# Kernel optimization log

Hardware: AMD Instinct MI355X
Metric: run time of the kernel (lower is better)

## Reference

```python
import jax, jax.numpy as jnp
import numpy as np
from jax.ops import segment_sum

N_NODES = 50000
N_EDGES = 800000
D_IN = 256
D_HID2 = 256   # hidden_channels * 2
D_HID = 128    # hidden_channels
D_MLP = 64     # hidden_channels // 2
D_OUT = 64


def setup_inputs() -> dict:
    key = jax.random.key(0)
    ks = jax.random.split(key, 16)
    def glorot(k, shape):
        lim = float(np.sqrt(6.0 / (shape[0] + shape[1])))
        return jax.random.uniform(k, shape, jnp.float32, -lim, lim)
    x = jax.random.normal(ks[0], (N_NODES, D_IN), jnp.float32)
    edge_index = jax.random.randint(ks[1], (2, N_EDGES), 0, N_NODES, jnp.int64)
    return {
        "x": x,
        "edge_index": edge_index,
        "W1": glorot(ks[2], (D_IN, D_HID2)),   "b1": jnp.zeros((D_HID2,), jnp.float32),
        "W2": glorot(ks[3], (D_HID2, D_HID2)), "b2": jnp.zeros((D_HID2,), jnp.float32),
        "W3": glorot(ks[4], (D_HID2, D_HID)),  "b3": jnp.zeros((D_HID,), jnp.float32),
        "mW1": glorot(ks[5], (D_HID, D_MLP)),  "mb1": jnp.zeros((D_MLP,), jnp.float32),
        "mW2": glorot(ks[6], (D_MLP, D_OUT)),  "mb2": jnp.zeros((D_OUT,), jnp.float32),
    }


def _graph_conv(x, src, dst, W, b, n_nodes):
    # DGL GraphConv with norm='both': h = D_in^{-1/2} * A @ (D_out^{-1/2} * x @ W) + b
    ones = jnp.ones((src.shape[0],), x.dtype)
    deg_out = jnp.clip(segment_sum(ones, src, num_segments=n_nodes), 1.0)
    deg_in = jnp.clip(segment_sum(ones, dst, num_segments=n_nodes), 1.0)
    h = (x * jax.lax.rsqrt(deg_out)[:, None]) @ W          # [N, d_out]
    agg = segment_sum(h[src], dst, num_segments=n_nodes)    # gather-scatter over edges
    return agg * jax.lax.rsqrt(deg_in)[:, None] + b


def reference(x, edge_index, W1, b1, W2, b2, W3, b3, mW1, mb1, mW2, mb2):
    src, dst = edge_index[0], edge_index[1]
    n = x.shape[0]
    # eval mode: dropout is identity
    h = jax.nn.relu(_graph_conv(x, src, dst, W1, b1, n))
    h = jax.nn.relu(_graph_conv(h, src, dst, W2, b2, n))
    h_last = jax.nn.relu(_graph_conv(h, src, dst, W3, b3, n))
    out = jax.nn.relu(h_last @ mW1 + mb1) @ mW2 + mb2
    return (out, h_last)
```

## Files before the change

### kernel.cpp

```cpp
#include <hip/hip_runtime.h>
#include <hip/hip_bf16.h>

typedef __hip_bfloat16 bf16;
typedef __attribute__((ext_vector_type(8))) __bf16 bfrag;
typedef __attribute__((ext_vector_type(4))) float f32x4;

#define N_NODES 50000
#define N_EDGES 800000
#define GB_GEMM 782
#define GB_PLACE 3125

__device__ __forceinline__ unsigned short f2bf(float f) {
    bf16 h = __float2bfloat16(f);
    return *reinterpret_cast<unsigned short*>(&h);
}

__device__ __forceinline__ uint4 zero4() { uint4 z; z.x = z.y = z.z = z.w = 0u; return z; }

__device__ __forceinline__ void load_edge(const int* __restrict__ ei, int fl64,
                                          int e, int& s, int& d) {
    if (fl64) {
        int2 a = ((const int2*)ei)[e];
        int2 b = ((const int2*)ei)[N_EDGES + e];
        s = a.x; d = b.x;
    } else {
        s = ei[e];
        d = ei[N_EDGES + e];
    }
}

__device__ __forceinline__ float rdf(const void* p, int off, int f32) {
    return f32 ? ((const float*)p)[off] : (float)((const bf16*)p)[off];
}

__global__ void detect_zero_kernel(const unsigned short* __restrict__ xb,
                                   const int* __restrict__ ei,
                                   int* __restrict__ flags,
                                   int* __restrict__ cnt) {
    int i = blockIdx.x * 256 + threadIdx.x;
    if (i < 2 * N_NODES) cnt[i] = 0;
    if (blockIdx.x == 0) {
        __shared__ int s_insane, s_nonzero;
        int t = threadIdx.x;
        if (t == 0) { s_insane = 0; s_nonzero = 0; }
        __syncthreads();
        unsigned short h = xb[2 * t];
        int e = (h >> 7) & 0xFF;
        if (!(e == 0 || (e >= 90 && e <= 150))) atomicOr(&s_insane, 1);
        if (ei[2 * t + 1] != 0) atomicOr(&s_nonzero, 1);
        __syncthreads();
        if (t == 0) { flags[0] = s_insane ? 1 : 0; flags[1] = s_nonzero ? 0 : 1; }
    }
}

__global__ void cvt_all_kernel(const void* W1, const void* W2, const void* W3,
                               const void* mW1, const void* mW2,
                               const void* b1, const void* b2, const void* b3,
                               const void* mb1, const void* mb2,
                               const int* __restrict__ flags,
                               unsigned short* __restrict__ WT,
                               float* __restrict__ biasd) {
    int i = blockIdx.x * 256 + threadIdx.x;
    if (i >= 176896) return;
    const int f32 = flags[0];
    if (i < 163840) {
        const void* s; int local, N;
        if      (i <  65536) { s = W1; local = i;          N = 256; }
        else if (i < 131072) { s = W2; local = i -  65536; N = 256; }
        else                 { s = W3; local = i - 131072; N = 128; }
        int n = local >> 8, k = local & 255;
        WT[i] = f2bf(rdf(s, k * N + n, f32));
    } else if (i < 172032) {
        int local = i - 163840;
        int n = local >> 7, k = local & 127;
        WT[i] = f2bf(rdf(mW1, k * 64 + n, f32));
    } else if (i < 176128) {
        int local = i - 172032;
        int n = local >> 6, k = local & 63;
        WT[i] = f2bf(rdf(mW2, k * 64 + n, f32));
    } else {
        int local = i - 176128;
        const void* s; int off;
        if      (local < 256) { s = b1;  off = local; }
        else if (local < 512) { s = b2;  off = local - 256; }
        else if (local < 640) { s = b3;  off = local - 512; }
        else if (local < 704) { s = mb1; off = local - 640; }
        else                  { s = mb2; off = local - 704; }
        biasd[local] = rdf(s, off, f32);
    }
}

__device__ __forceinline__ uint4 ld8_bf16(const unsigned short* p) {
    return *(const uint4*)p;
}
__device__ __forceinline__ uint4 ld8_f32(const float* p) {
    float4 a = *(const float4*)(p);
    float4 b = *(const float4*)(p + 4);
    uint4 r;
    r.x = ((unsigned)f2bf(a.y) << 16) | f2bf(a.x);
    r.y = ((unsigned)f2bf(a.w) << 16) | f2bf(a.z);
    r.z = ((unsigned)f2bf(b.y) << 16) | f2bf(b.x);
    r.w = ((unsigned)f2bf(b.w) << 16) | f2bf(b.z);
    return r;
}

template <bool DUALX, bool PRESCALE>
__device__ __forceinline__ void gemm_body(
        unsigned short (*Xs)[40], unsigned short (*Ws)[40],
        const void* __restrict__ Xv, const int* __restrict__ flags,
        const unsigned short* __restrict__ WT,
        const int* __restrict__ cntS,
        unsigned short* __restrict__ C,
        int bx, int by, int M, int N) {
    constexpr int K = 256;
    const int tid  = threadIdx.x;
    const int lane = tid & 63;
    const int w    = tid >> 6;
    const int wr   = (w >> 1) * 64;
    const int wc   = (w & 1) * 64;
    const int lrow = lane & 15;
    const int koff = (lane >> 4) * 8;
    const int row0 = by * 128;
    const int col0 = bx * 128;
    const bool xf32 = DUALX && (flags[0] != 0);
    const unsigned short* Xb = (const unsigned short*)Xv;
    const float* Xf = (const float*)Xv;

    const int r0 = tid >> 2, q0 = tid & 3;
    const int r1 = r0 + 64;
    const int gr0 = row0 + r0, gr1 = row0 + r1;

    uint4 xv0, xv1, wv0, wv1;
    {
        int e = q0 * 8;
        xv0 = (gr0 < M) ? (xf32 ? ld8_f32(Xf + (size_t)gr0 * K + e)
                                : ld8_bf16(Xb + (size_t)gr0 * K + e)) : zero4();
        xv1 = (gr1 < M) ? (xf32 ? ld8_f32(Xf + (size_t)gr1 * K + e)
                                : ld8_bf16(Xb + (size_t)gr1 * K + e)) : zero4();
        wv0 = *(const uint4*)(WT + (size_t)(col0 + r0) * K + e);
        wv1 = *(const uint4*)(WT + (size_t)(col0 + r1) * K + e);
    }

    f32x4 acc[4][4] = {};

    for (int k0 = 0; k0 < K; k0 += 32) {
        *(uint4*)&Xs[r0][q0 * 8] = xv0;
        *(uint4*)&Xs[r1][q0 * 8] = xv1;
        *(uint4*)&Ws[r0][q0 * 8] = wv0;
        *(uint4*)&Ws[r1][q0 * 8] = wv1;
        __syncthreads();

        const int k1 = k0 + 32;
        if (k1 < K) {
            int e = k1 + q0 * 8;
            xv0 = (gr0 < M) ? (xf32 ? ld8_f32(Xf + (size_t)gr0 * K + e)
                                    : ld8_bf16(Xb + (size_t)gr0 * K + e)) : zero4();
            xv1 = (gr1 < M) ? (xf32 ? ld8_f32(Xf + (size_t)gr1 * K + e)
                                    : ld8_bf16(Xb + (size_t)gr1 * K + e)) : zero4();
            wv0 = *(const uint4*)(WT + (size_t)(col0 + r0) * K + e);
            wv1 = *(const uint4*)(WT + (size_t)(col0 + r1) * K + e);
        }

        bfrag af[4], bv[4];
#pragma unroll
        for (int i = 0; i < 4; i++)
            af[i] = *(const bfrag*)&Xs[wr + i * 16 + lrow][koff];
#pragma unroll
        for (int j = 0; j < 4; j++)
            bv[j] = *(const bfrag*)&Ws[wc + j * 16 + lrow][koff];
#pragma unroll
        for (int i = 0; i < 4; i++)
#pragma unroll
            for (int j = 0; j < 4; j++)
                acc[i][j] = __builtin_amdgcn_mfma_f32_16x16x32_bf16(
                    af[i], bv[j], acc[i][j], 0, 0, 0);
        __syncthreads();
    }

#pragma unroll
    for (int i = 0; i < 4; i++) {
#pragma unroll
        for (int r = 0; r < 4; r++) {
            int row = row0 + wr + i * 16 + ((lane >> 4) * 4) + r;
            if (row >= M) continue;
            const float s = PRESCALE ? rsqrtf((float)max(cntS[row], 1)) : 1.0f;
#pragma unroll
            for (int j = 0; j < 4; j++) {
                int col = col0 + wc + j * 16 + lrow;
                C[(size_t)row * N + col] = f2bf(acc[i][j][r] * s);
            }
        }
    }
}

__launch_bounds__(256)
__global__ void megaA_kernel(const void* __restrict__ x,
                             const int* __restrict__ ei,
                             const int* __restrict__ flags,
                             const unsigned short* __restrict__ WT,
                             unsigned short* __restrict__ Hbf,
                             int* __restrict__ cntS, int* __restrict__ cntD,
                             unsigned short* __restrict__ esrc_pad, int M) {
    __shared__ unsigned short Xs[128][40];
    __shared__ unsigned short Ws[128][40];
    const int bid = blockIdx.x;
    if (bid < GB_PLACE) {
        int e = bid * 256 + threadIdx.x;
        if (e < N_EDGES) {
            int s, d; load_edge(ei, flags[1], e, s, d);
            atomicAdd(&cntS[s], 1);
            int pos = atomicAdd(&cntD[d], 1);
            if (pos < 64)
                __builtin_nontemporal_store((unsigned short)s,
                                            &esrc_pad[(d << 6) + pos]);
        }
    } else {
        const int gb = bid - GB_PLACE;
        gemm_body<true, false>(Xs, Ws, x, flags, WT, nullptr, Hbf,
                               gb & 1, gb >> 1, M, 256);
    }
}

__launch_bounds__(256)
__global__ void mfma_gemm_kernel(const unsigned short* __restrict__ X,
                                 const int* __restrict__ flags,
                                 const unsigned short* __restrict__ WT,
                                 const int* __restrict__ cntS,
                                 unsigned short* __restrict__ C,
                                 int M, int N) {
    __shared__ unsigned short Xs[128][40];
    __shared__ unsigned short Ws[128][40];
    gemm_body<false, true>(Xs, Ws, X, flags, WT, cntS, C,
                           blockIdx.x, blockIdx.y, M, N);
}

__launch_bounds__(256)
__global__ void mfma_mlp2_kernel(const unsigned short* __restrict__ X,
                                 const unsigned short* __restrict__ WT1,
                                 const unsigned short* __restrict__ WT2,
                                 const float* __restrict__ b1,
                                 const float* __restrict__ b2,
                                 float* __restrict__ out, int M) {
    __shared__ unsigned short Xs[128][136];
    __shared__ unsigned short W1s[64][136];
    __shared__ unsigned short W2s[64][72];
    const int tid  = threadIdx.x;
    const int lane = tid & 63;
    const int w    = tid >> 6;
    const int lrow = lane & 15;
    const int koff = (lane >> 4) * 8;
    const int row0 = blockIdx.x * 128;

#pragma unroll
    for (int i = 0; i < 8; i++) {
        int c = tid + i * 256;
        int r = c >> 4, q = c & 15;
        int gr = row0 + r;
        uint4 v = (gr < M) ? *(const uint4*)(X + (size_t)gr * 128 + q * 8) : zero4();
        *(uint4*)&Xs[r][q * 8] = v;
    }
#pragma unroll
    for (int i = 0; i < 4; i++) {
        int c = tid + i * 256;
        int n = c >> 4, q = c & 15;
        *(uint4*)&W1s[n][q * 8] = *(const uint4*)(WT1 + (size_t)n * 128 + q * 8);
    }
#pragma unroll
    for (int i = 0; i < 2; i++) {
        int c = tid + i * 256;
        int n = c >> 3, q = c & 7;
        *(uint4*)&W2s[n][q * 8] = *(const uint4*)(WT2 + (size_t)n * 64 + q * 8);
    }
    __syncthreads();

    f32x4 acc[2][4] = {};
#pragma unroll
    for (int k0 = 0; k0 < 128; k0 += 32) {
        bfrag af[2], bv[4];
#pragma unroll
        for (int i = 0; i < 2; i++)
            af[i] = *(const bfrag*)&Xs[w * 32 + i * 16 + lrow][k0 + koff];
#pragma unroll
        for (int j = 0; j < 4; j++)
            bv[j] = *(const bfrag*)&W1s[j * 16 + lrow][k0 + koff];
#pragma unroll
        for (int i = 0; i < 2; i++)
#pragma unroll
            for (int j = 0; j < 4; j++)
                acc[i][j] = __builtin_amdgcn_mfma_f32_16x16x32_bf16(
                    af[i], bv[j], acc[i][j], 0, 0, 0);
    }
    __syncthreads();

#pragma unroll
    for (int i = 0; i < 2; i++) {
#pragma unroll
        for (int r = 0; r < 4; r++) {
            int row = w * 32 + i * 16 + ((lane >> 4) * 4) + r;
#pragma unroll
            for (int j = 0; j < 4; j++) {
                int col = j * 16 + lrow;
                Xs[row][col] = f2bf(fmaxf(acc[i][j][r] + b1[col], 0.0f));
            }
        }
    }
    __syncthreads();

    f32x4 acc2[2][4] = {};
#pragma unroll
    for (int k0 = 0; k0 < 64; k0 += 32) {
        bfrag af[2], bv[4];
#pragma unroll
        for (int i = 0; i < 2; i++)
            af[i] = *(const bfrag*)&Xs[w * 32 + i * 16 + lrow][k0 + koff];
#pragma unroll
        for (int j = 0; j < 4; j++)
            bv[j] = *(const bfrag*)&W2s[j * 16 + lrow][k0 + koff];
#pragma unroll
        for (int i = 0; i < 2; i++)
#pragma unroll
            for (int j = 0; j < 4; j++)
                acc2[i][j] = __builtin_amdgcn_mfma_f32_16x16x32_bf16(
                    af[i], bv[j], acc2[i][j], 0, 0, 0);
    }

#pragma unroll
    for (int i = 0; i < 2; i++) {
#pragma unroll
        for (int r = 0; r < 4; r++) {
            int row = row0 + w * 32 + i * 16 + ((lane >> 4) * 4) + r;
            if (row >= M) continue;
#pragma unroll
            for (int j = 0; j < 4; j++) {
                int col = j * 16 + lrow;
                out[(size_t)row * 64 + col] = acc2[i][j][r] + b2[col];
            }
        }
    }
}

__device__ __forceinline__ void accs(unsigned int u, float s, float& a0, float& a1) {
    a0 = fmaf(s, __uint_as_float(u << 16), a0);
    a1 = fmaf(s, __uint_as_float(u & 0xffff0000u), a1);
}
__device__ __forceinline__ void acc4s(uint4 u, float s, float (&a)[8]) {
    accs(u.x, s, a[0], a[1]); accs(u.y, s, a[2], a[3]);
    accs(u.z, s, a[4], a[5]); accs(u.w, s, a[6], a[7]);
}

template <int LQ, bool ESCALE, int OUT>
__launch_bounds__(256)
__global__ void gather_bf16_kernel(const int* __restrict__ cntD,
                                   const int* __restrict__ cntS,
                                   const unsigned short* __restrict__ esrc_pad,
                                   const unsigned short* __restrict__ H,
                                   const float* __restrict__ bias,
                                   float* __restrict__ Yf,
                                   unsigned short* __restrict__ Yb, int nNodes) {
    constexpr int NPB = 256 / LQ;
    constexpr int D = LQ * 8;
    const int tid = threadIdx.x;
    const int node = blockIdx.x * NPB + tid / LQ;
    const int lane = tid % LQ;
    if (node >= nNodes) return;
    const uint4* __restrict__ H4 = (const uint4*)H;
    const unsigned short* __restrict__ ep = esrc_pad + (node << 6);

    float a[8] = {};
    const int cn = min(cntD[node], 64);
    int j = 0;
    for (; j + 8 <= cn; j += 8) {
        int s[8];
#pragma unroll
        for (int t = 0; t < 8; t++) s[t] = ep[j + t];
        float w[8];
#pragma unroll
        for (int t = 0; t < 8; t++)
            w[t] = ESCALE ? rsqrtf((float)max(cntS[s[t]], 1)) : 1.0f;
        uint4 u[8];
#pragma unroll
        for (int t = 0; t < 8; t++) u[t] = H4[(size_t)s[t] * LQ + lane];
#pragma unroll
        for (int t = 0; t < 8; t++) acc4s(u[t], w[t], a);
    }
    for (; j + 4 <= cn; j += 4) {
        int s[4];
#pragma unroll
        for (int t = 0; t < 4; t++) s[t] = ep[j + t];
        float w[4];
#pragma unroll
        for (int t = 0; t < 4; t++)
            w[t] = ESCALE ? rsqrtf((float)max(cntS[s[t]], 1)) : 1.0f;
        uint4 u[4];
#pragma unroll
        for (int t = 0; t < 4; t++) u[t] = H4[(size_t)s[t] * LQ + lane];
#pragma unroll
        for (int t = 0; t < 4; t++) acc4s(u[t], w[t], a);
    }
    for (; j < cn; j++) {
        int s0 = ep[j];
        float w0 = ESCALE ? rsqrtf((float)max(cntS[s0], 1)) : 1.0f;
        uint4 u = H4[(size_t)s0 * LQ + lane];
        acc4s(u, w0, a);
    }
    const float sc = rsqrtf((float)max(cntD[node], 1));
    const float* bp = bias + lane * 8;
    float4 b0 = *(const float4*)(bp);
    float4 b1 = *(const float4*)(bp + 4);
    float r0 = fmaxf(fmaf(a[0], sc, b0.x), 0.0f);
    float r1 = fmaxf(fmaf(a[1], sc, b0.y), 0.0f);
    float r2 = fmaxf(fmaf(a[2], sc, b0.z), 0.0f);
    float r3 = fmaxf(fmaf(a[3], sc, b0.w), 0.0f);
    float r4 = fmaxf(fmaf(a[4], sc, b1.x), 0.0f);
    float r5 = fmaxf(fmaf(a[5], sc, b1.y), 0.0f);
    float r6 = fmaxf(fmaf(a[6], sc, b1.z), 0.0f);
    float r7 = fmaxf(fmaf(a[7], sc, b1.w), 0.0f);
    if (OUT == 2) {
        float* yp = Yf + (size_t)node * D + lane * 8;
        float4 o0 = {r0, r1, r2, r3};
        float4 o1 = {r4, r5, r6, r7};
        *(float4*)(yp)     = o0;
        *(float4*)(yp + 4) = o1;
    }
    {
        unsigned short* yp = Yb + (size_t)node * D + lane * 8;
        ushort4 o0, o1;
        o0.x = f2bf(r0); o0.y = f2bf(r1); o0.z = f2bf(r2); o0.w = f2bf(r3);
        o1.x = f2bf(r4); o1.y = f2bf(r5); o1.z = f2bf(r6); o1.w = f2bf(r7);
        *(ushort4*)(yp)     = o0;
        *(ushort4*)(yp + 4) = o1;
    }
}

extern "C" void kernel_launch(void* const* d_in, const int* in_sizes, int n_in,
                              void* d_out, int out_size, void* d_ws, size_t ws_size,
                              hipStream_t stream) {
    const void* x  = d_in[0];
    const int*  ei = (const int*)d_in[1];
    const void *W1 = d_in[2],  *b1 = d_in[3];
    const void *W2 = d_in[4],  *b2 = d_in[5];
    const void *W3 = d_in[6],  *b3 = d_in[7];
    const void *mW1 = d_in[8], *mb1 = d_in[9];
    const void *mW2 = d_in[10],*mb2 = d_in[11];

    float* out   = (float*)d_out;
    float* out_h = out + (size_t)N_NODES * 64;

    float* ws = (float*)d_ws;
    size_t off = 0;
    int*   flags  = (int*)(ws + off); off += 64;
    int*   cntS   = (int*)(ws + off); off += N_NODES;
    int*   cntD   = (int*)(ws + off); off += N_NODES;
    unsigned short* esrc_p = (unsigned short*)(ws + off);
    off += (size_t)N_NODES * 32;
    float* biasd  = ws + off;         off += 768;
    off = (off + 63) & ~(size_t)63;
    unsigned short* WT  = (unsigned short*)(ws + off); off += 88448;
    unsigned short* Gbf = (unsigned short*)(ws + off); off += (size_t)N_NODES * 128;
    unsigned short* Hbf = (unsigned short*)(ws + off); off += (size_t)N_NODES * 128;
    unsigned short* hob = (unsigned short*)(ws + off); off += (size_t)N_NODES * 64;

    const int M = N_NODES;
    const dim3 blk(256);
    const int gy128 = (M + 127) / 128;

    detect_zero_kernel<<<391, blk, 0, stream>>>(
        (const unsigned short*)x, ei, flags, cntS);

    cvt_all_kernel<<<(176896 + 255) / 256, blk, 0, stream>>>(
        W1, W2, W3, mW1, mW2, b1, b2, b3, mb1, mb2, flags, WT, biasd);

    megaA_kernel<<<GB_GEMM + GB_PLACE, blk, 0, stream>>>(
        x, ei, flags, WT, Hbf, cntS, cntD, esrc_p, M);

    gather_bf16_kernel<32, true, 0><<<(M + 7) / 8, blk, 0, stream>>>(
        cntD, cntS, esrc_p, Hbf, biasd, nullptr, Gbf, M);

    mfma_gemm_kernel<<<dim3(2, gy128), blk, 0, stream>>>(
        Gbf, flags, WT + 65536, cntS, Hbf, M, 256);
    gather_bf16_kernel<32, false, 0><<<(M + 7) / 8, blk, 0, stream>>>(
        cntD, cntS, esrc_p, Hbf, biasd + 256, nullptr, Gbf, M);

    mfma_gemm_kernel<<<dim3(1, gy128), blk, 0, stream>>>(
        Gbf, flags, WT + 131072, cntS, Hbf, M, 128);
    gather_bf16_kernel<16, false, 2><<<(M + 15) / 16, blk, 0, stream>>>(
        cntD, cntS, esrc_p, Hbf, biasd + 512, out_h, hob, M);

    mfma_mlp2_kernel<<<gy128, blk, 0, stream>>>(
        hob, WT + 163840, WT + 172032, biasd + 640, biasd + 704, out, M);
}
```

Before: 418.2 us.

## Split gather/GEMM stages by row range and co-schedule tails with next stage

Each gather stage is split at row 40960. The head rows are gathered first. The tail-row gather then runs in the same launch as the GEMM blocks for the first 320 row tiles, whose inputs are already complete. The remaining GEMM tiles run in a separate launch afterwards. The goal is to fill the idle tail of each dependent stage and overlap gather with matmul. The change also reorders megaA so the GEMM blocks are dispatched before the edge-placement blocks, and it reuses the out_h region as scratch for H2. This adds launches and depends on exact block-count bookkeeping, and H2 lives in output memory that is overwritten later.

```diff
diff --git a/kernel.cpp b/kernel.cpp
--- a/kernel.cpp
+++ b/kernel.cpp
@@ -9,6 +9,8 @@
 #define N_EDGES 800000
 #define GB_GEMM 782
 #define GB_PLACE 3125
+#define RSPLIT 40960
+#define NTAIL (N_NODES - RSPLIT)
 
 __device__ __forceinline__ unsigned short f2bf(float f) {
     bf16 h = __float2bfloat16(f);
@@ -204,8 +206,11 @@
     __shared__ unsigned short Xs[128][40];
     __shared__ unsigned short Ws[128][40];
     const int bid = blockIdx.x;
-    if (bid < GB_PLACE) {
-        int e = bid * 256 + threadIdx.x;
+    if (bid < GB_GEMM) {
+        gemm_body<true, false>(Xs, Ws, x, flags, WT, nullptr, Hbf,
+                               bid & 1, bid >> 1, M, 256);
+    } else {
+        int e = (bid - GB_GEMM) * 256 + threadIdx.x;
         if (e < N_EDGES) {
             int s, d; load_edge(ei, flags[1], e, s, d);
             atomicAdd(&cntS[s], 1);
@@ -214,128 +219,6 @@
                 __builtin_nontemporal_store((unsigned short)s,
                                             &esrc_pad[(d << 6) + pos]);
         }
-    } else {
-        const int gb = bid - GB_PLACE;
-        gemm_body<true, false>(Xs, Ws, x, flags, WT, nullptr, Hbf,
-                               gb & 1, gb >> 1, M, 256);
-    }
-}
-
-__launch_bounds__(256)
-__global__ void mfma_gemm_kernel(const unsigned short* __restrict__ X,
-                                 const int* __restrict__ flags,
-                                 const unsigned short* __restrict__ WT,
-                                 const int* __restrict__ cntS,
-                                 unsigned short* __restrict__ C,
-                                 int M, int N) {
-    __shared__ unsigned short Xs[128][40];
-    __shared__ unsigned short Ws[128][40];
-    gemm_body<false, true>(Xs, Ws, X, flags, WT, cntS, C,
-                           blockIdx.x, blockIdx.y, M, N);
-}
-
-__launch_bounds__(256)
-__global__ void mfma_mlp2_kernel(const unsigned short* __restrict__ X,
-                                 const unsigned short* __restrict__ WT1,
-                                 const unsigned short* __restrict__ WT2,
-                                 const float* __restrict__ b1,
-                                 const float* __restrict__ b2,
-                                 float* __restrict__ out, int M) {
-    __shared__ unsigned short Xs[128][136];
-    __shared__ unsigned short W1s[64][136];
-    __shared__ unsigned short W2s[64][72];
-    const int tid  = threadIdx.x;
-    const int lane = tid & 63;
-    const int w    = tid >> 6;
-    const int lrow = lane & 15;
-    const int koff = (lane >> 4) * 8;
-    const int row0 = blockIdx.x * 128;
-
-#pragma unroll
-    for (int i = 0; i < 8; i++) {
-        int c = tid + i * 256;
-        int r = c >> 4, q = c & 15;
-        int gr = row0 + r;
-        uint4 v = (gr < M) ? *(const uint4*)(X + (size_t)gr * 128 + q * 8) : zero4();
-        *(uint4*)&Xs[r][q * 8] = v;
-    }
-#pragma unroll
-    for (int i = 0; i < 4; i++) {
-        int c = tid + i * 256;
-        int n = c >> 4, q = c & 15;
-        *(uint4*)&W1s[n][q * 8] = *(const uint4*)(WT1 + (size_t)n * 128 + q * 8);
-    }
-#pragma unroll
-    for (int i = 0; i < 2; i++) {
-        int c = tid + i * 256;
-        int n = c >> 3, q = c & 7;
-        *(uint4*)&W2s[n][q * 8] = *(const uint4*)(WT2 + (size_t)n * 64 + q * 8);
-    }
-    __syncthreads();
-
-    f32x4 acc[2][4] = {};
-#pragma unroll
-    for (int k0 = 0; k0 < 128; k0 += 32) {
-        bfrag af[2], bv[4];
-#pragma unroll
-        for (int i = 0; i < 2; i++)
-            af[i] = *(const bfrag*)&Xs[w * 32 + i * 16 + lrow][k0 + koff];
-#pragma unroll
-        for (int j = 0; j < 4; j++)
-            bv[j] = *(const bfrag*)&W1s[j * 16 + lrow][k0 + koff];
-#pragma unroll
-        for (int i = 0; i < 2; i++)
-#pragma unroll
-            for (int j = 0; j < 4; j++)
-                acc[i][j] = __builtin_amdgcn_mfma_f32_16x16x32_bf16(
-                    af[i], bv[j], acc[i][j], 0, 0, 0);
-    }
-    __syncthreads();
-
-#pragma unroll
-    for (int i = 0; i < 2; i++) {
-#pragma unroll
-        for (int r = 0; r < 4; r++) {
-            int row = w * 32 + i * 16 + ((lane >> 4) * 4) + r;
-#pragma unroll
-            for (int j = 0; j < 4; j++) {
-                int col = j * 16 + lrow;
-                Xs[row][col] = f2bf(fmaxf(acc[i][j][r] + b1[col], 0.0f));
-            }
-        }
-    }
-    __syncthreads();
-
-    f32x4 acc2[2][4] = {};
-#pragma unroll
-    for (int k0 = 0; k0 < 64; k0 += 32) {
-        bfrag af[2], bv[4];
-#pragma unroll
-        for (int i = 0; i < 2; i++)
-            af[i] = *(const bfrag*)&Xs[w * 32 + i * 16 + lrow][k0 + koff];
-#pragma unroll
-        for (int j = 0; j < 4; j++)
-            bv[j] = *(const bfrag*)&W2s[j * 16 + lrow][k0 + koff];
-#pragma unroll
-        for (int i = 0; i < 2; i++)
-#pragma unroll
-            for (int j = 0; j < 4; j++)
-                acc2[i][j] = __builtin_amdgcn_mfma_f32_16x16x32_bf16(
-                    af[i], bv[j], acc2[i][j], 0, 0, 0);
-    }
-
-#pragma unroll
-    for (int i = 0; i < 2; i++) {
-#pragma unroll
-        for (int r = 0; r < 4; r++) {
-            int row = row0 + w * 32 + i * 16 + ((lane >> 4) * 4) + r;
-            if (row >= M) continue;
-#pragma unroll
-            for (int j = 0; j < 4; j++) {
-                int col = j * 16 + lrow;
-                out[(size_t)row * 64 + col] = acc2[i][j][r] + b2[col];
-            }
-        }
     }
 }
 
@@ -349,20 +232,15 @@
 }
 
 template <int LQ, bool ESCALE, int OUT>
-__launch_bounds__(256)
-__global__ void gather_bf16_kernel(const int* __restrict__ cntD,
-                                   const int* __restrict__ cntS,
-                                   const unsigned short* __restrict__ esrc_pad,
-                                   const unsigned short* __restrict__ H,
-                                   const float* __restrict__ bias,
-                                   float* __restrict__ Yf,
-                                   unsigned short* __restrict__ Yb, int nNodes) {
-    constexpr int NPB = 256 / LQ;
+__device__ __forceinline__ void gather_body(const int* __restrict__ cntD,
+                                            const int* __restrict__ cntS,
+                                            const unsigned short* __restrict__ esrc_pad,
+                                            const unsigned short* __restrict__ H,
+                                            const float* __restrict__ bias,
+                                            float* __restrict__ Yf,
+                                            unsigned short* __restrict__ Yb,
+                                            int node, int lane) {
     constexpr int D = LQ * 8;
-    const int tid = threadIdx.x;
-    const int node = blockIdx.x * NPB + tid / LQ;
-    const int lane = tid % LQ;
-    if (node >= nNodes) return;
     const uint4* __restrict__ H4 = (const uint4*)H;
     const unsigned short* __restrict__ ep = esrc_pad + (node << 6);
 
@@ -432,6 +310,234 @@
     }
 }
 
+template <int LQ, bool ESCALE, int OUT>
+__launch_bounds__(256)
+__global__ void gather_bf16_kernel(const int* __restrict__ cntD,
+                                   const int* __restrict__ cntS,
+                                   const unsigned short* __restrict__ esrc_pad,
+                                   const unsigned short* __restrict__ H,
+                                   const float* __restrict__ bias,
+                                   float* __restrict__ Yf,
+                                   unsigned short* __restrict__ Yb,
+                                   int n0, int n1) {
+    constexpr int NPB = 256 / LQ;
+    const int node = n0 + blockIdx.x * NPB + threadIdx.x / LQ;
+    const int lane = threadIdx.x % LQ;
+    if (node >= n1) return;
+    gather_body<LQ, ESCALE, OUT>(cntD, cntS, esrc_pad, H, bias, Yf, Yb, node, lane);
+}
+
+#define MB_G 1130
+__launch_bounds__(256)
+__global__ void megaB_kernel(const int* __restrict__ cntD,
+                             const int* __restrict__ cntS,
+                             const unsigned short* __restrict__ esrc_pad,
+                             const unsigned short* __restrict__ Hbf,
+                             const float* __restrict__ biasd,
+                             unsigned short* __restrict__ Gbf,
+                             const int* __restrict__ flags,
+                             const unsigned short* __restrict__ WT2,
+                             unsigned short* __restrict__ H2, int M) {
+    const int bid = blockIdx.x;
+    if (bid < MB_G) {
+        const int node = RSPLIT + bid * 8 + threadIdx.x / 32;
+        const int lane = threadIdx.x % 32;
+        if (node >= M) return;
+        gather_body<32, true, 0>(cntD, cntS, esrc_pad, Hbf, biasd,
+                                 nullptr, Gbf, node, lane);
+    } else {
+        __shared__ unsigned short Xs[128][40];
+        __shared__ unsigned short Ws[128][40];
+        const int gb = bid - MB_G;
+        gemm_body<false, true>(Xs, Ws, Gbf, flags, WT2, cntS, H2,
+                               gb & 1, gb >> 1, M, 256);
+    }
+}
+
+__launch_bounds__(256)
+__global__ void megaC_kernel(const int* __restrict__ cntD,
+                             const int* __restrict__ cntS,
+                             const unsigned short* __restrict__ esrc_pad,
+                             const unsigned short* __restrict__ H2,
+                             const float* __restrict__ bias2,
+                             unsigned short* __restrict__ Gbf,
+                             const int* __restrict__ flags,
+                             const unsigned short* __restrict__ WT3,
+                             unsigned short* __restrict__ H3, int M) {
+    const int bid = blockIdx.x;
+    if (bid < MB_G) {
+        const int node = RSPLIT + bid * 8 + threadIdx.x / 32;
+        const int lane = threadIdx.x % 32;
+        if (node >= M) return;
+        gather_body<32, false, 0>(cntD, cntS, esrc_pad, H2, bias2,
+                                  nullptr, Gbf, node, lane);
+    } else {
+        __shared__ unsigned short Xs[128][40];
+        __shared__ unsigned short Ws[128][40];
+        const int gb = bid - MB_G;
+        gemm_body<false, true>(Xs, Ws, Gbf, flags, WT3, cntS, H3,
+                               0, gb, M, 128);
+    }
+}
+
+__launch_bounds__(256)
+__global__ void mfma_gemm_kernel(const unsigned short* __restrict__ X,
+                                 const int* __restrict__ flags,
+                                 const unsigned short* __restrict__ WT,
+                                 const int* __restrict__ cntS,
+                                 unsigned short* __restrict__ C,
+                                 int M, int N, int by0) {
+    __shared__ unsigned short Xs[128][40];
+    __shared__ unsigned short Ws[128][40];
+    gemm_body<false, true>(Xs, Ws, X, flags, WT, cntS, C,
+                           blockIdx.x, by0 + blockIdx.y, M, N);
+}
+
+__device__ __forceinline__ void mlp2_body(
+        unsigned short (*Xs)[136], unsigned short (*W1s)[136],
+        unsigned short (*W2s)[72],
+        const unsigned short* __restrict__ X,
+        const unsigned short* __restrict__ WT1,
+        const unsigned short* __restrict__ WT2,
+        const float* __restrict__ b1, const float* __restrict__ b2,
+        float* __restrict__ out, int M, int row0) {
+    const int tid  = threadIdx.x;
+    const int lane = tid & 63;
+    const int w    = tid >> 6;
+    const int lrow = lane & 15;
+    const int koff = (lane >> 4) * 8;
+
+#pragma unroll
+    for (int i = 0; i < 8; i++) {
+        int c = tid + i * 256;
+        int r = c >> 4, q = c & 15;
+        int gr = row0 + r;
+        uint4 v = (gr < M) ? *(const uint4*)(X + (size_t)gr * 128 + q * 8) : zero4();
+        *(uint4*)&Xs[r][q * 8] = v;
+    }
+#pragma unroll
+    for (int i = 0; i < 4; i++) {
+        int c = tid + i * 256;
+        int n = c >> 4, q = c & 15;
+        *(uint4*)&W1s[n][q * 8] = *(const uint4*)(WT1 + (size_t)n * 128 + q * 8);
+    }
+#pragma unroll
+    for (int i = 0; i < 2; i++) {
+        int c = tid + i * 256;
+        int n = c >> 3, q = c & 7;
+        *(uint4*)&W2s[n][q * 8] = *(const uint4*)(WT2 + (size_t)n * 64 + q * 8);
+    }
+    __syncthreads();
+
+    f32x4 acc[2][4] = {};
+#pragma unroll
+    for (int k0 = 0; k0 < 128; k0 += 32) {
+        bfrag af[2], bv[4];
+#pragma unroll
+        for (int i = 0; i < 2; i++)
+            af[i] = *(const bfrag*)&Xs[w * 32 + i * 16 + lrow][k0 + koff];
+#pragma unroll
+        for (int j = 0; j < 4; j++)
+            bv[j] = *(const bfrag*)&W1s[j * 16 + lrow][k0 + koff];
+#pragma unroll
+        for (int i = 0; i < 2; i++)
+#pragma unroll
+            for (int j = 0; j < 4; j++)
+                acc[i][j] = __builtin_amdgcn_mfma_f32_16x16x32_bf16(
+                    af[i], bv[j], acc[i][j], 0, 0, 0);
+    }
+    __syncthreads();
+
+#pragma unroll
+    for (int i = 0; i < 2; i++) {
+#pragma unroll
+        for (int r = 0; r < 4; r++) {
+            int row = w * 32 + i * 16 + ((lane >> 4) * 4) + r;
+#pragma unroll
+            for (int j = 0; j < 4; j++) {
+                int col = j * 16 + lrow;
+                Xs[row][col] = f2bf(fmaxf(acc[i][j][r] + b1[col], 0.0f));
+            }
+        }
+    }
+    __syncthreads();
+
+    f32x4 acc2[2][4] = {};
+#pragma unroll
+    for (int k0 = 0; k0 < 64; k0 += 32) {
+        bfrag af[2], bv[4];
+#pragma unroll
+        for (int i = 0; i < 2; i++)
+            af[i] = *(const bfrag*)&Xs[w * 32 + i * 16 + lrow][k0 + koff];
+#pragma unroll
+        for (int j = 0; j < 4; j++)
+            bv[j] = *(const bfrag*)&W2s[j * 16 + lrow][k0 + koff];
+#pragma unroll
+        for (int i = 0; i < 2; i++)
+#pragma unroll
+            for (int j = 0; j < 4; j++)
+                acc2[i][j] = __builtin_amdgcn_mfma_f32_16x16x32_bf16(
+                    af[i], bv[j], acc2[i][j], 0, 0, 0);
+    }
+
+#pragma unroll
+    for (int i = 0; i < 2; i++) {
+#pragma unroll
+        for (int r = 0; r < 4; r++) {
+            int row = row0 + w * 32 + i * 16 + ((lane >> 4) * 4) + r;
+            if (row >= M) continue;
+#pragma unroll
+            for (int j = 0; j < 4; j++) {
+                int col = j * 16 + lrow;
+                out[(size_t)row * 64 + col] = acc2[i][j][r] + b2[col];
+            }
+        }
+    }
+}
+
+__launch_bounds__(256)
+__global__ void mfma_mlp2_kernel(const unsigned short* __restrict__ X,
+                                 const unsigned short* __restrict__ WT1,
+                                 const unsigned short* __restrict__ WT2,
+                                 const float* __restrict__ b1,
+                                 const float* __restrict__ b2,
+                                 float* __restrict__ out, int M, int tile0) {
+    __shared__ unsigned short Xs[128][136];
+    __shared__ unsigned short W1s[64][136];
+    __shared__ unsigned short W2s[64][72];
+    mlp2_body(Xs, W1s, W2s, X, WT1, WT2, b1, b2, out, M,
+              (tile0 + blockIdx.x) * 128);
+}
+
+#define MD_G 565
+__launch_bounds__(256)
+__global__ void megaD_kernel(const int* __restrict__ cntD,
+                             const unsigned short* __restrict__ esrc_pad,
+                             const unsigned short* __restrict__ H3,
+                             const float* __restrict__ bias3,
+                             float* __restrict__ outh,
+                             unsigned short* __restrict__ hob,
+                             const unsigned short* __restrict__ WT1,
+                             const unsigned short* __restrict__ WT2,
+                             const float* __restrict__ mb1,
+                             const float* __restrict__ mb2,
+                             float* __restrict__ out, int M) {
+    const int bid = blockIdx.x;
+    if (bid < MD_G) {
+        const int node = RSPLIT + bid * 16 + threadIdx.x / 16;
+        const int lane = threadIdx.x % 16;
+        if (node >= M) return;
+        gather_body<16, false, 2>(cntD, nullptr, esrc_pad, H3, bias3,
+                                  outh, hob, node, lane);
+    } else {
+        __shared__ unsigned short Xs[128][136];
+        __shared__ unsigned short W1s[64][136];
+        __shared__ unsigned short W2s[64][72];
+        mlp2_body(Xs, W1s, W2s, hob, WT1, WT2, mb1, mb2, out, M,
+                  (bid - MD_G) * 128);
+    }
+}
+
 extern "C" void kernel_launch(void* const* d_in, const int* in_sizes, int n_in,
                               void* d_out, int out_size, void* d_ws, size_t ws_size,
                               hipStream_t stream) {
@@ -459,10 +565,11 @@
     unsigned short* Gbf = (unsigned short*)(ws + off); off += (size_t)N_NODES * 128;
     unsigned short* Hbf = (unsigned short*)(ws + off); off += (size_t)N_NODES * 128;
     unsigned short* hob = (unsigned short*)(ws + off); off += (size_t)N_NODES * 64;
+    unsigned short* H2 = (unsigned short*)out_h;
+    unsigned short* H3 = Hbf;
 
     const int M = N_NODES;
     const dim3 blk(256);
-    const int gy128 = (M + 127) / 128;
 
     detect_zero_kernel<<<391, blk, 0, stream>>>(
         (const unsigned short*)x, ei, flags, cntS);
@@ -473,19 +580,31 @@
     megaA_kernel<<<GB_GEMM + GB_PLACE, blk, 0, stream>>>(
         x, ei, flags, WT, Hbf, cntS, cntD, esrc_p, M);
 
-    gather_bf16_kernel<32, true, 0><<<(M + 7) / 8, blk, 0, stream>>>(
-        cntD, cntS, esrc_p, Hbf, biasd, nullptr, Gbf, M);
-
-    mfma_gemm_kernel<<<dim3(2, gy128), blk, 0, stream>>>(
-        Gbf, flags, WT + 65536, cntS, Hbf, M, 256);
-    gather_bf16_kernel<32, false, 0><<<(M + 7) / 8, blk, 0, stream>>>(
-        cntD, cntS, esrc_p, Hbf, biasd + 256, nullptr, Gbf, M);
-
-    mfma_gemm_kernel<<<dim3(1, gy128), blk, 0, stream>>>(
-        Gbf, flags, WT + 131072, cntS, Hbf, M, 128);
-    gather_bf16_kernel<16, false, 2><<<(M + 15) / 16, blk, 0, stream>>>(
-        cntD, cntS, esrc_p, Hbf, biasd + 512, out_h, hob, M);
-
-    mfma_mlp2_kernel<<<gy128, blk, 0, stream>>>(
-        hob, WT + 163840, WT + 172032, biasd + 640, biasd + 704, out, M);
-}
+    gather_bf16_kernel<32, true, 0><<<RSPLIT / 8, blk, 0, stream>>>(
+        cntD, cntS, esrc_p, Hbf, biasd, nullptr, Gbf, 0, RSPLIT);
+
+    megaB_kernel<<<MB_G + 640, blk, 0, stream>>>(
+        cntD, cntS, esrc_p, Hbf, biasd, Gbf, flags, WT + 65536, H2, M);
+
+    mfma_gemm_kernel<<<dim3(2, 71), blk, 0, stream>>>(
+        Gbf, flags, WT + 65536, cntS, H2, M, 256, 320);
+
+    gather_bf16_kernel<32, false, 0><<<RSPLIT / 8, blk, 0, stream>>>(
+        cntD, cntS, esrc_p, H2, biasd + 256, nullptr, Gbf, 0, RSPLIT);
+
+    megaC_kernel<<<MB_G + 320, blk, 0, stream>>>(
+        cntD, cntS, esrc_p, H2, biasd + 256, Gbf, flags, WT + 131072, H3, M);
+
+    mfma_gemm_kernel<<<dim3(1, 71), blk, 0, stream>>>(
+        Gbf, flags, WT + 131072, cntS, H3, M, 128, 320);
+
+    gather_bf16_kernel<16, false, 2><<<RSPLIT / 16, blk, 0, stream>>>(
+        cntD, nullptr, esrc_p, H3, biasd + 512, out_h, hob, 0, RSPLIT);
+
+    megaD_kernel<<<MD_G + 320, blk, 0, stream>>>(
+        cntD, esrc_p, H3, biasd + 512, out_h, hob,
+        WT + 163840, WT + 172032, biasd + 640, biasd + 704, out, M);
+
+    mfma_mlp2_kernel<<<71, blk, 0, stream>>>(
+        hob, WT + 163840, WT + 172032, biasd + 640, biasd + 704, out, M, 320);
+}
```

Result: no change. 422.7 us (+1.1%).

## Sort per-node neighbor lists and gather in source-row tiles for cache locality

Applied to the files above, without the earlier changes.

Adds a wave-level bitonic sort of each destination node's padded source list. The gather is replaced by a tiled version in which each thread group handles 8 nodes and sweeps source rows in windows, so concurrent groups touch the same H rows and reuse them in L2. It also reorders megaA so GEMM blocks are scheduled before the edge-placement blocks. The cost is an extra sort kernel, many more loop iterations over tiles, register pressure from 8 accumulators per thread, and far fewer blocks per gather launch.

```diff
diff --git a/kernel.cpp b/kernel.cpp
--- a/kernel.cpp
+++ b/kernel.cpp
@@ -204,8 +204,11 @@
     __shared__ unsigned short Xs[128][40];
     __shared__ unsigned short Ws[128][40];
     const int bid = blockIdx.x;
-    if (bid < GB_PLACE) {
-        int e = bid * 256 + threadIdx.x;
+    if (bid < GB_GEMM) {
+        gemm_body<true, false>(Xs, Ws, x, flags, WT, nullptr, Hbf,
+                               bid & 1, bid >> 1, M, 256);
+    } else {
+        int e = (bid - GB_GEMM) * 256 + threadIdx.x;
         if (e < N_EDGES) {
             int s, d; load_edge(ei, flags[1], e, s, d);
             atomicAdd(&cntS[s], 1);
@@ -214,10 +217,135 @@
                 __builtin_nontemporal_store((unsigned short)s,
                                             &esrc_pad[(d << 6) + pos]);
         }
-    } else {
-        const int gb = bid - GB_PLACE;
-        gemm_body<true, false>(Xs, Ws, x, flags, WT, nullptr, Hbf,
-                               gb & 1, gb >> 1, M, 256);
+    }
+}
+
+__launch_bounds__(256)
+__global__ void sort_kernel(const int* __restrict__ cntD,
+                            unsigned short* __restrict__ esrc_pad, int nNodes) {
+    const int node = blockIdx.x * 4 + (threadIdx.x >> 6);
+    const int lane = threadIdx.x & 63;
+    if (node >= nNodes) return;
+    unsigned short* ep = esrc_pad + (node << 6);
+    const int cn = min(cntD[node], 64);
+    unsigned v = (lane < cn) ? (unsigned)ep[lane] : 0xFFFFu;
+#pragma unroll
+    for (int k = 2; k <= 64; k <<= 1) {
+#pragma unroll
+        for (int m = k >> 1; m >= 1; m >>= 1) {
+            unsigned p = __shfl_xor(v, m, 64);
+            bool lower = (lane & m) == 0;
+            bool asc   = (lane & k) == 0;
+            unsigned lo = v < p ? v : p;
+            unsigned hi = v < p ? p : v;
+            v = (asc == lower) ? lo : hi;
+        }
+    }
+    if (lane < cn) ep[lane] = (unsigned short)v;
+}
+
+__device__ __forceinline__ void accs(unsigned int u, float s, float& a0, float& a1) {
+    a0 = fmaf(s, __uint_as_float(u << 16), a0);
+    a1 = fmaf(s, __uint_as_float(u & 0xffff0000u), a1);
+}
+__device__ __forceinline__ void acc4s(uint4 u, float s, float (&a)[8]) {
+    accs(u.x, s, a[0], a[1]); accs(u.y, s, a[2], a[3]);
+    accs(u.z, s, a[4], a[5]); accs(u.w, s, a[6], a[7]);
+}
+
+template <int LQ, bool ESCALE, int OUT, int TROWS>
+__launch_bounds__(256)
+__global__ void gather_tiled_kernel(const int* __restrict__ cntD,
+                                    const int* __restrict__ cntS,
+                                    const unsigned short* __restrict__ esrc_pad,
+                                    const unsigned short* __restrict__ H,
+                                    const float* __restrict__ bias,
+                                    float* __restrict__ Yf,
+                                    unsigned short* __restrict__ Yb, int M) {
+    constexpr int NPG = 8;
+    constexpr int GPB = 256 / LQ;
+    constexpr int D = LQ * 8;
+    const int g    = blockIdx.x * GPB + threadIdx.x / LQ;
+    const int lane = threadIdx.x % LQ;
+    const int node0 = g * NPG;
+    if (node0 >= M) return;
+    const uint4* __restrict__ H4 = (const uint4*)H;
+
+    float acc[NPG][8] = {};
+    int ptr[NPG], cn[NPG];
+#pragma unroll
+    for (int i = 0; i < NPG; i++) {
+        const int nd = node0 + i;
+        cn[i] = (nd < M) ? min(cntD[nd], 64) : 0;
+        ptr[i] = 0;
+    }
+
+    for (int t0 = 0; t0 < M; t0 += TROWS) {
+        const int tEnd = t0 + TROWS;
+#pragma unroll
+        for (int i = 0; i < NPG; i++) {
+            const unsigned short* ep = esrc_pad + ((size_t)(node0 + i) << 6);
+            int j = ptr[i];
+            const int c = cn[i];
+            while (j + 4 <= c) {
+                const int s0 = ep[j], s1 = ep[j + 1], s2 = ep[j + 2], s3 = ep[j + 3];
+                if (s3 >= tEnd) break;
+                float w0 = 1.f, w1 = 1.f, w2 = 1.f, w3 = 1.f;
+                if (ESCALE) {
+                    w0 = rsqrtf((float)max(cntS[s0], 1));
+                    w1 = rsqrtf((float)max(cntS[s1], 1));
+                    w2 = rsqrtf((float)max(cntS[s2], 1));
+                    w3 = rsqrtf((float)max(cntS[s3], 1));
+                }
+                uint4 u0 = H4[(size_t)s0 * LQ + lane];
+                uint4 u1 = H4[(size_t)s1 * LQ + lane];
+                uint4 u2 = H4[(size_t)s2 * LQ + lane];
+                uint4 u3 = H4[(size_t)s3 * LQ + lane];
+                acc4s(u0, w0, acc[i]); acc4s(u1, w1, acc[i]);
+                acc4s(u2, w2, acc[i]); acc4s(u3, w3, acc[i]);
+                j += 4;
+            }
+            while (j < c) {
+                const int s0 = ep[j];
+                if (s0 >= tEnd) break;
+                const float w0 = ESCALE ? rsqrtf((float)max(cntS[s0], 1)) : 1.f;
+                uint4 u = H4[(size_t)s0 * LQ + lane];
+                acc4s(u, w0, acc[i]);
+                j++;
+            }
+            ptr[i] = j;
+        }
+    }
+
+#pragma unroll
+    for (int i = 0; i < NPG; i++) {
+        const int nd = node0 + i;
+        if (nd >= M) continue;
+        const float sc = rsqrtf((float)max(cntD[nd], 1));
+        const float* bp = bias + lane * 8;
+        float4 b0 = *(const float4*)(bp);
+        float4 b1 = *(const float4*)(bp + 4);
+        float r0 = fmaxf(fmaf(acc[i][0], sc, b0.x), 0.0f);
+        float r1 = fmaxf(fmaf(acc[i][1], sc, b0.y), 0.0f);
+        float r2 = fmaxf(fmaf(acc[i][2], sc, b0.z), 0.0f);
+        float r3 = fmaxf(fmaf(acc[i][3], sc, b0.w), 0.0f);
+        float r4 = fmaxf(fmaf(acc[i][4], sc, b1.x), 0.0f);
+        float r5 = fmaxf(fmaf(acc[i][5], sc, b1.y), 0.0f);
+        float r6 = fmaxf(fmaf(acc[i][6], sc, b1.z), 0.0f);
+        float r7 = fmaxf(fmaf(acc[i][7], sc, b1.w), 0.0f);
+        if (OUT == 2) {
+            float* yp = Yf + (size_t)nd * D + lane * 8;
+            float4 o0 = {r0, r1, r2, r3};
+            float4 o1 = {r4, r5, r6, r7};
+            *(float4*)(yp)     = o0;
+            *(float4*)(yp + 4) = o1;
+        }
+        unsigned short* yp = Yb + (size_t)nd * D + lane * 8;
+        ushort4 o0, o1;
+        o0.x = f2bf(r0); o0.y = f2bf(r1); o0.z = f2bf(r2); o0.w = f2bf(r3);
+        o1.x = f2bf(r4); o1.y = f2bf(r5); o1.z = f2bf(r6); o1.w = f2bf(r7);
+        *(ushort4*)(yp)     = o0;
+        *(ushort4*)(yp + 4) = o1;
     }
 }
 
@@ -339,99 +467,6 @@
     }
 }
 
-__device__ __forceinline__ void accs(unsigned int u, float s, float& a0, float& a1) {
-    a0 = fmaf(s, __uint_as_float(u << 16), a0);
-    a1 = fmaf(s, __uint_as_float(u & 0xffff0000u), a1);
-}
-__device__ __forceinline__ void acc4s(uint4 u, float s, float (&a)[8]) {
-    accs(u.x, s, a[0], a[1]); accs(u.y, s, a[2], a[3]);
-    accs(u.z, s, a[4], a[5]); accs(u.w, s, a[6], a[7]);
-}
-
-template <int LQ, bool ESCALE, int OUT>
-__launch_bounds__(256)
-__global__ void gather_bf16_kernel(const int* __restrict__ cntD,
-                                   const int* __restrict__ cntS,
-                                   const unsigned short* __restrict__ esrc_pad,
-                                   const unsigned short* __restrict__ H,
-                                   const float* __restrict__ bias,
-                                   float* __restrict__ Yf,
-                                   unsigned short* __restrict__ Yb, int nNodes) {
-    constexpr int NPB = 256 / LQ;
-    constexpr int D = LQ * 8;
-    const int tid = threadIdx.x;
-    const int node = blockIdx.x * NPB + tid / LQ;
-    const int lane = tid % LQ;
-    if (node >= nNodes) return;
-    const uint4* __restrict__ H4 = (const uint4*)H;
-    const unsigned short* __restrict__ ep = esrc_pad + (node << 6);
-
-    float a[8] = {};
-    const int cn = min(cntD[node], 64);
-    int j = 0;
-    for (; j + 8 <= cn; j += 8) {
-        int s[8];
-#pragma unroll
-        for (int t = 0; t < 8; t++) s[t] = ep[j + t];
-        float w[8];
-#pragma unroll
-        for (int t = 0; t < 8; t++)
-            w[t] = ESCALE ? rsqrtf((float)max(cntS[s[t]], 1)) : 1.0f;
-        uint4 u[8];
-#pragma unroll
-        for (int t = 0; t < 8; t++) u[t] = H4[(size_t)s[t] * LQ + lane];
-#pragma unroll
-        for (int t = 0; t < 8; t++) acc4s(u[t], w[t], a);
-    }
-    for (; j + 4 <= cn; j += 4) {
-        int s[4];
-#pragma unroll
-        for (int t = 0; t < 4; t++) s[t] = ep[j + t];
-        float w[4];
-#pragma unroll
-        for (int t = 0; t < 4; t++)
-            w[t] = ESCALE ? rsqrtf((float)max(cntS[s[t]], 1)) : 1.0f;
-        uint4 u[4];
-#pragma unroll
-        for (int t = 0; t < 4; t++) u[t] = H4[(size_t)s[t] * LQ + lane];
-#pragma unroll
-        for (int t = 0; t < 4; t++) acc4s(u[t], w[t], a);
-    }
-    for (; j < cn; j++) {
-        int s0 = ep[j];
-        float w0 = ESCALE ? rsqrtf((float)max(cntS[s0], 1)) : 1.0f;
-        uint4 u = H4[(size_t)s0 * LQ + lane];
-        acc4s(u, w0, a);
-    }
-    const float sc = rsqrtf((float)max(cntD[node], 1));
-    const float* bp = bias + lane * 8;
-    float4 b0 = *(const float4*)(bp);
-    float4 b1 = *(const float4*)(bp + 4);
-    float r0 = fmaxf(fmaf(a[0], sc, b0.x), 0.0f);
-    float r1 = fmaxf(fmaf(a[1], sc, b0.y), 0.0f);
-    float r2 = fmaxf(fmaf(a[2], sc, b0.z), 0.0f);
-    float r3 = fmaxf(fmaf(a[3], sc, b0.w), 0.0f);
-    float r4 = fmaxf(fmaf(a[4], sc, b1.x), 0.0f);
-    float r5 = fmaxf(fmaf(a[5], sc, b1.y), 0.0f);
-    float r6 = fmaxf(fmaf(a[6], sc, b1.z), 0.0f);
-    float r7 = fmaxf(fmaf(a[7], sc, b1.w), 0.0f);
-    if (OUT == 2) {
-        float* yp = Yf + (size_t)node * D + lane * 8;
-        float4 o0 = {r0, r1, r2, r3};
-        float4 o1 = {r4, r5, r6, r7};
-        *(float4*)(yp)     = o0;
-        *(float4*)(yp + 4) = o1;
-    }
-    {
-        unsigned short* yp = Yb + (size_t)node * D + lane * 8;
-        ushort4 o0, o1;
-        o0.x = f2bf(r0); o0.y = f2bf(r1); o0.z = f2bf(r2); o0.w = f2bf(r3);
-        o1.x = f2bf(r4); o1.y = f2bf(r5); o1.z = f2bf(r6); o1.w = f2bf(r7);
-        *(ushort4*)(yp)     = o0;
-        *(ushort4*)(yp + 4) = o1;
-    }
-}
-
 extern "C" void kernel_launch(void* const* d_in, const int* in_sizes, int n_in,
                               void* d_out, int out_size, void* d_ws, size_t ws_size,
                               hipStream_t stream) {
@@ -473,18 +508,20 @@
     megaA_kernel<<<GB_GEMM + GB_PLACE, blk, 0, stream>>>(
         x, ei, flags, WT, Hbf, cntS, cntD, esrc_p, M);
 
-    gather_bf16_kernel<32, true, 0><<<(M + 7) / 8, blk, 0, stream>>>(
+    sort_kernel<<<(M + 3) / 4, blk, 0, stream>>>(cntD, esrc_p, M);
+
+    gather_tiled_kernel<32, true, 0, 6144><<<782, blk, 0, stream>>>(
         cntD, cntS, esrc_p, Hbf, biasd, nullptr, Gbf, M);
 
     mfma_gemm_kernel<<<dim3(2, gy128), blk, 0, stream>>>(
         Gbf, flags, WT + 65536, cntS, Hbf, M, 256);
-    gather_bf16_kernel<32, false, 0><<<(M + 7) / 8, blk, 0, stream>>>(
+    gather_tiled_kernel<32, false, 0, 6144><<<782, blk, 0, stream>>>(
         cntD, cntS, esrc_p, Hbf, biasd + 256, nullptr, Gbf, M);
 
     mfma_gemm_kernel<<<dim3(1, gy128), blk, 0, stream>>>(
         Gbf, flags, WT + 131072, cntS, Hbf, M, 128);
-    gather_bf16_kernel<16, false, 2><<<(M + 15) / 16, blk, 0, stream>>>(
-        cntD, cntS, esrc_p, Hbf, biasd + 512, out_h, hob, M);
+    gather_tiled_kernel<16, false, 2, 12288><<<391, blk, 0, stream>>>(
+        cntD, nullptr, esrc_p, Hbf, biasd + 512, out_h, hob, M);
 
     mfma_mlp2_kernel<<<gy128, blk, 0, stream>>>(
         hob, WT + 163840, WT + 172032, biasd + 640, biasd + 704, out, M);
```

Result: slower. 885.8 us (+111.8%).

## Split gather into feature-half passes and reorder megaA gemm/placement blocks

Applied to the files above, without the earlier changes.

Rewrites the neighbor-aggregation kernel so each pass gathers only half of each feature row, with twice as many blocks covering nodes in two column-half passes. The intent is to shrink the working set of gathered H rows per pass so it fits better in cache, and to raise parallelism per node. The cost is that edge lists, degree counts and scale factors are read twice, and the inner loop unroll drops from 8 to 4. Separately, megaA now dispatches GEMM blocks before the edge-placement blocks, which may change how the two kinds of work overlap.

```diff
diff --git a/kernel.cpp b/kernel.cpp
--- a/kernel.cpp
+++ b/kernel.cpp
@@ -204,8 +204,11 @@
     __shared__ unsigned short Xs[128][40];
     __shared__ unsigned short Ws[128][40];
     const int bid = blockIdx.x;
-    if (bid < GB_PLACE) {
-        int e = bid * 256 + threadIdx.x;
+    if (bid < GB_GEMM) {
+        gemm_body<true, false>(Xs, Ws, x, flags, WT, nullptr, Hbf,
+                               bid & 1, bid >> 1, M, 256);
+    } else {
+        int e = (bid - GB_GEMM) * 256 + threadIdx.x;
         if (e < N_EDGES) {
             int s, d; load_edge(ei, flags[1], e, s, d);
             atomicAdd(&cntS[s], 1);
@@ -214,10 +217,91 @@
                 __builtin_nontemporal_store((unsigned short)s,
                                             &esrc_pad[(d << 6) + pos]);
         }
-    } else {
-        const int gb = bid - GB_PLACE;
-        gemm_body<true, false>(Xs, Ws, x, flags, WT, nullptr, Hbf,
-                               gb & 1, gb >> 1, M, 256);
+    }
+}
+
+__device__ __forceinline__ void accs(unsigned int u, float s, float& a0, float& a1) {
+    a0 = fmaf(s, __uint_as_float(u << 16), a0);
+    a1 = fmaf(s, __uint_as_float(u & 0xffff0000u), a1);
+}
+__device__ __forceinline__ void acc4s(uint4 u, float s, float (&a)[8]) {
+    accs(u.x, s, a[0], a[1]); accs(u.y, s, a[2], a[3]);
+    accs(u.z, s, a[4], a[5]); accs(u.w, s, a[6], a[7]);
+}
+
+template <int LQ, bool ESCALE, int OUT, int DFULL>
+__launch_bounds__(256)
+__global__ void gather_half_kernel(const int* __restrict__ cntD,
+                                   const int* __restrict__ cntS,
+                                   const unsigned short* __restrict__ esrc_pad,
+                                   const unsigned short* __restrict__ H,
+                                   const float* __restrict__ bias,
+                                   float* __restrict__ Yf,
+                                   unsigned short* __restrict__ Yb,
+                                   int M, int nblk_per_pass) {
+    constexpr int NPB = 256 / LQ;
+    constexpr int RQ  = DFULL / 8;
+    const int half = blockIdx.x / nblk_per_pass;
+    const int nb   = blockIdx.x - half * nblk_per_pass;
+    const int node = nb * NPB + threadIdx.x / LQ;
+    const int lane = threadIdx.x % LQ;
+    if (node >= M) return;
+    const uint4* __restrict__ H4 = (const uint4*)H;
+    const unsigned short* __restrict__ ep = esrc_pad + (node << 6);
+    const int qoff = half * LQ + lane;
+
+    float a[8] = {};
+    const int cn = min(cntD[node], 64);
+    int j = 0;
+    for (; j + 4 <= cn; j += 4) {
+        int s0 = ep[j], s1 = ep[j + 1], s2 = ep[j + 2], s3 = ep[j + 3];
+        float w0 = 1.f, w1 = 1.f, w2 = 1.f, w3 = 1.f;
+        if (ESCALE) {
+            w0 = rsqrtf((float)max(cntS[s0], 1));
+            w1 = rsqrtf((float)max(cntS[s1], 1));
+            w2 = rsqrtf((float)max(cntS[s2], 1));
+            w3 = rsqrtf((float)max(cntS[s3], 1));
+        }
+        uint4 u0 = H4[(size_t)s0 * RQ + qoff];
+        uint4 u1 = H4[(size_t)s1 * RQ + qoff];
+        uint4 u2 = H4[(size_t)s2 * RQ + qoff];
+        uint4 u3 = H4[(size_t)s3 * RQ + qoff];
+        acc4s(u0, w0, a); acc4s(u1, w1, a);
+        acc4s(u2, w2, a); acc4s(u3, w3, a);
+    }
+    for (; j < cn; j++) {
+        int s0 = ep[j];
+        float w0 = ESCALE ? rsqrtf((float)max(cntS[s0], 1)) : 1.0f;
+        uint4 u = H4[(size_t)s0 * RQ + qoff];
+        acc4s(u, w0, a);
+    }
+    const float sc = rsqrtf((float)max(cntD[node], 1));
+    const int colb = half * LQ * 8 + lane * 8;
+    const float* bp = bias + colb;
+    float4 b0 = *(const float4*)(bp);
+    float4 b1 = *(const float4*)(bp + 4);
+    float r0 = fmaxf(fmaf(a[0], sc, b0.x), 0.0f);
+    float r1 = fmaxf(fmaf(a[1], sc, b0.y), 0.0f);
+    float r2 = fmaxf(fmaf(a[2], sc, b0.z), 0.0f);
+    float r3 = fmaxf(fmaf(a[3], sc, b0.w), 0.0f);
+    float r4 = fmaxf(fmaf(a[4], sc, b1.x), 0.0f);
+    float r5 = fmaxf(fmaf(a[5], sc, b1.y), 0.0f);
+    float r6 = fmaxf(fmaf(a[6], sc, b1.z), 0.0f);
+    float r7 = fmaxf(fmaf(a[7], sc, b1.w), 0.0f);
+    if (OUT == 2) {
+        float* yp = Yf + (size_t)node * DFULL + colb;
+        float4 o0 = {r0, r1, r2, r3};
+        float4 o1 = {r4, r5, r6, r7};
+        *(float4*)(yp)     = o0;
+        *(float4*)(yp + 4) = o1;
+    }
+    {
+        unsigned short* yp = Yb + (size_t)node * DFULL + colb;
+        ushort4 o0, o1;
+        o0.x = f2bf(r0); o0.y = f2bf(r1); o0.z = f2bf(r2); o0.w = f2bf(r3);
+        o1.x = f2bf(r4); o1.y = f2bf(r5); o1.z = f2bf(r6); o1.w = f2bf(r7);
+        *(ushort4*)(yp)     = o0;
+        *(ushort4*)(yp + 4) = o1;
     }
 }
 
@@ -339,99 +423,6 @@
     }
 }
 
-__device__ __forceinline__ void accs(unsigned int u, float s, float& a0, float& a1) {
-    a0 = fmaf(s, __uint_as_float(u << 16), a0);
-    a1 = fmaf(s, __uint_as_float(u & 0xffff0000u), a1);
-}
-__device__ __forceinline__ void acc4s(uint4 u, float s, float (&a)[8]) {
-    accs(u.x, s, a[0], a[1]); accs(u.y, s, a[2], a[3]);
-    accs(u.z, s, a[4], a[5]); accs(u.w, s, a[6], a[7]);
-}
-
-template <int LQ, bool ESCALE, int OUT>
-__launch_bounds__(256)
-__global__ void gather_bf16_kernel(const int* __restrict__ cntD,
-                                   const int* __restrict__ cntS,
-                                   const unsigned short* __restrict__ esrc_pad,
-                                   const unsigned short* __restrict__ H,
-                                   const float* __restrict__ bias,
-                                   float* __restrict__ Yf,
-                                   unsigned short* __restrict__ Yb, int nNodes) {
-    constexpr int NPB = 256 / LQ;
-    constexpr int D = LQ * 8;
-    const int tid = threadIdx.x;
-    const int node = blockIdx.x * NPB + tid / LQ;
-    const int lane = tid % LQ;
-    if (node >= nNodes) return;
-    const uint4* __restrict__ H4 = (const uint4*)H;
-    const unsigned short* __restrict__ ep = esrc_pad + (node << 6);
-
-    float a[8] = {};
-    const int cn = min(cntD[node], 64);
-    int j = 0;
-    for (; j + 8 <= cn; j += 8) {
-        int s[8];
-#pragma unroll
-        for (int t = 0; t < 8; t++) s[t] = ep[j + t];
-        float w[8];
-#pragma unroll
-        for (int t = 0; t < 8; t++)
-            w[t] = ESCALE ? rsqrtf((float)max(cntS[s[t]], 1)) : 1.0f;
-        uint4 u[8];
-#pragma unroll
-        for (int t = 0; t < 8; t++) u[t] = H4[(size_t)s[t] * LQ + lane];
-#pragma unroll
-        for (int t = 0; t < 8; t++) acc4s(u[t], w[t], a);
-    }
-    for (; j + 4 <= cn; j += 4) {
-        int s[4];
-#pragma unroll
-        for (int t = 0; t < 4; t++) s[t] = ep[j + t];
-        float w[4];
-#pragma unroll
-        for (int t = 0; t < 4; t++)
-            w[t] = ESCALE ? rsqrtf((float)max(cntS[s[t]], 1)) : 1.0f;
-        uint4 u[4];
-#pragma unroll
-        for (int t = 0; t < 4; t++) u[t] = H4[(size_t)s[t] * LQ + lane];
-#pragma unroll
-        for (int t = 0; t < 4; t++) acc4s(u[t], w[t], a);
-    }
-    for (; j < cn; j++) {
-        int s0 = ep[j];
-        float w0 = ESCALE ? rsqrtf((float)max(cntS[s0], 1)) : 1.0f;
-        uint4 u = H4[(size_t)s0 * LQ + lane];
-        acc4s(u, w0, a);
-    }
-    const float sc = rsqrtf((float)max(cntD[node], 1));
-    const float* bp = bias + lane * 8;
-    float4 b0 = *(const float4*)(bp);
-    float4 b1 = *(const float4*)(bp + 4);
-    float r0 = fmaxf(fmaf(a[0], sc, b0.x), 0.0f);
-    float r1 = fmaxf(fmaf(a[1], sc, b0.y), 0.0f);
-    float r2 = fmaxf(fmaf(a[2], sc, b0.z), 0.0f);
-    float r3 = fmaxf(fmaf(a[3], sc, b0.w), 0.0f);
-    float r4 = fmaxf(fmaf(a[4], sc, b1.x), 0.0f);
-    float r5 = fmaxf(fmaf(a[5], sc, b1.y), 0.0f);
-    float r6 = fmaxf(fmaf(a[6], sc, b1.z), 0.0f);
-    float r7 = fmaxf(fmaf(a[7], sc, b1.w), 0.0f);
-    if (OUT == 2) {
-        float* yp = Yf + (size_t)node * D + lane * 8;
-        float4 o0 = {r0, r1, r2, r3};
-        float4 o1 = {r4, r5, r6, r7};
-        *(float4*)(yp)     = o0;
-        *(float4*)(yp + 4) = o1;
-    }
-    {
-        unsigned short* yp = Yb + (size_t)node * D + lane * 8;
-        ushort4 o0, o1;
-        o0.x = f2bf(r0); o0.y = f2bf(r1); o0.z = f2bf(r2); o0.w = f2bf(r3);
-        o1.x = f2bf(r4); o1.y = f2bf(r5); o1.z = f2bf(r6); o1.w = f2bf(r7);
-        *(ushort4*)(yp)     = o0;
-        *(ushort4*)(yp + 4) = o1;
-    }
-}
-
 extern "C" void kernel_launch(void* const* d_in, const int* in_sizes, int n_in,
                               void* d_out, int out_size, void* d_ws, size_t ws_size,
                               hipStream_t stream) {
@@ -473,18 +464,18 @@
     megaA_kernel<<<GB_GEMM + GB_PLACE, blk, 0, stream>>>(
         x, ei, flags, WT, Hbf, cntS, cntD, esrc_p, M);
 
-    gather_bf16_kernel<32, true, 0><<<(M + 7) / 8, blk, 0, stream>>>(
-        cntD, cntS, esrc_p, Hbf, biasd, nullptr, Gbf, M);
+    gather_half_kernel<16, true, 0, 256><<<6250, blk, 0, stream>>>(
+        cntD, cntS, esrc_p, Hbf, biasd, nullptr, Gbf, M, 3125);
 
     mfma_gemm_kernel<<<dim3(2, gy128), blk, 0, stream>>>(
         Gbf, flags, WT + 65536, cntS, Hbf, M, 256);
-    gather_bf16_kernel<32, false, 0><<<(M + 7) / 8, blk, 0, stream>>>(
-        cntD, cntS, esrc_p, Hbf, biasd + 256, nullptr, Gbf, M);
+    gather_half_kernel<16, false, 0, 256><<<6250, blk, 0, stream>>>(
+        cntD, cntS, esrc_p, Hbf, biasd + 256, nullptr, Gbf, M, 3125);
 
     mfma_gemm_kernel<<<dim3(1, gy128), blk, 0, stream>>>(
         Gbf, flags, WT + 131072, cntS, Hbf, M, 128);
-    gather_bf16_kernel<16, false, 2><<<(M + 15) / 16, blk, 0, stream>>>(
-        cntD, cntS, esrc_p, Hbf, biasd + 512, out_h, hob, M);
+    gather_half_kernel<8, false, 2, 128><<<3126, blk, 0, stream>>>(
+        cntD, nullptr, esrc_p, Hbf, biasd + 512, out_h, hob, M, 1563);
 
     mfma_mlp2_kernel<<<gy128, blk, 0, stream>>>(
         hob, WT + 163840, WT + 172032, biasd + 640, biasd + 704, out, M);
```

After: 389.6 us. 6.8% less time.
